# Kernel tuning notes

Measured on AMD Instinct MI355X. Metric: run time of the kernel, lower is better.

The kernel has to match this reference:

```python
import jax, jax.numpy as jnp
import numpy as np

DIM = 224   # channels, divisible by shift_size
SHIFT = 7   # shift_sizes[0]
PAD = 3     # shift_size // 2 (matches hardcoded F.pad of 3)
B, D, H, W = 2, 32, 32, 32
EPS = 1e-5


def setup_inputs() -> dict:
    key = jax.random.key(0)
    ks = jax.random.split(key, 12)
    w = lambda k: jax.random.normal(k, (DIM, DIM), jnp.float32) * 0.02
    b = lambda k: jax.random.normal(k, (DIM,), jnp.float32) * 0.02
    return {
        "x": jax.random.normal(ks[0], (B, DIM, D, H, W), jnp.float32),
        "conv1_w": w(ks[1]), "conv1_b": b(ks[2]),
        "conv21_w": w(ks[3]), "conv21_b": b(ks[4]),
        "conv22_w": w(ks[5]), "conv22_b": b(ks[6]),
        "conv23_w": w(ks[7]), "conv23_b": b(ks[8]),
        "conv3_w": w(ks[9]), "conv3_b": b(ks[10]),
        "n1_g": jnp.ones((DIM,), jnp.float32), "n1_b": jnp.zeros((DIM,), jnp.float32),
        "n2_g": jnp.ones((DIM,), jnp.float32), "n2_b": jnp.zeros((DIM,), jnp.float32),
    }


def _pw(x, w, b):
    # 1x1x1 conv3d == per-voxel channel GEMM
    return jnp.einsum('bcdhw,oc->bodhw', x, w) + b[None, :, None, None, None]


def _gn(x, g, b):
    # GroupNorm(1, C): normalize over (C,D,H,W) per sample, per-channel affine
    mu = jnp.mean(x, axis=(1, 2, 3, 4), keepdims=True)
    var = jnp.mean((x - mu) ** 2, axis=(1, 2, 3, 4), keepdims=True)
    xn = (x - mu) * jax.lax.rsqrt(var + EPS)
    return xn * g[None, :, None, None, None] + b[None, :, None, None, None]


def _pad3(x):
    return jnp.pad(x, ((0, 0), (0, 0), (PAD, PAD), (PAD, PAD), (PAD, PAD)))


def _shift_narrow(xp, axis):
    # chunk channels into SHIFT groups, roll each by -PAD..PAD along `axis`,
    # concat, then narrow each spatial dim at offset PAD to (D,H,W)
    chunks = jnp.split(xp, SHIFT, axis=1)
    rolled = [jnp.roll(c, s, axis=axis) for c, s in zip(chunks, range(-PAD, PAD + 1))]
    cat = jnp.concatenate(rolled, axis=1)
    return cat[:, :, PAD:PAD + D, PAD:PAD + H, PAD:PAD + W]


def reference(x, conv1_w, conv1_b, conv21_w, conv21_b, conv22_w, conv22_b,
              conv23_w, conv23_b, conv3_w, conv3_b, n1_g, n1_b, n2_g, n2_b):
    gelu = lambda t: jax.nn.gelu(t, approximate=False)
    x_orig = x
    h = gelu(_gn(_pw(x, conv1_w, conv1_b), n1_g, n1_b))
    # NOTE: torch code re-pads the running tensor before each axis branch,
    # while always narrowing at offset PAD — reproduced faithfully.
    xp1 = _pad3(h)                       # padded once
    x_d = gelu(_pw(_shift_narrow(xp1, 2), conv21_w, conv21_b))
    xp2 = _pad3(xp1)                     # padded twice
    x_h = gelu(_pw(_shift_narrow(xp2, 3), conv22_w, conv22_b))
    xp3 = _pad3(xp2)                     # padded thrice
    x_w = gelu(_pw(_shift_narrow(xp3, 4), conv23_w, conv23_b))
    y = _pw(_gn(x_d + x_h + x_w, n2_g, n2_b), conv3_w, conv3_b)
    return y + x_orig
```

## Files before the change

### kernel.cpp

```cpp
#include <hip/hip_runtime.h>

#define DIM 224
#define NVOX 32768
#define NBATCH 2

typedef __attribute__((ext_vector_type(8))) short bf16x8;
typedef __attribute__((ext_vector_type(4))) float f32x4;

__device__ __forceinline__ unsigned short f2bf(float f){
  unsigned int u = __builtin_bit_cast(unsigned int, f);
  u += 0x7fffu + ((u >> 16) & 1u);
  return (unsigned short)(u >> 16);
}
__device__ __forceinline__ float bf2f(unsigned short s){
  unsigned int u = ((unsigned int)s) << 16;
  return __builtin_bit_cast(float, u);
}
__device__ __forceinline__ float gelu_f(float x){
  return 0.5f * x * (1.0f + erff(x * 0.70710678118654752440f));
}

__device__ __forceinline__ void gemm_core(const unsigned short* Atile,
                                          unsigned short* Wtile,
                                          const unsigned short* __restrict__ wmat,
                                          int tid, int lane, int wm, int wn,
                                          f32x4 acc[2][7])
{
  for (int ks = 0; ks < 7; ++ks){
    if (ks) __syncthreads();
    #pragma unroll
    for (int it = 0; it < 4; ++it){
      int idx = tid + it * 256;
      if (idx < 896){
        int o = idx >> 2, kp = idx & 3;
        *(bf16x8*)&Wtile[o * 40 + kp * 8] =
            *(const bf16x8*)&wmat[o * 224 + ks * 32 + kp * 8];
      }
    }
    __syncthreads();
    bf16x8 af[2];
    #pragma unroll
    for (int m = 0; m < 2; ++m){
      int row = wm * 32 + m * 16 + (lane & 15);
      int up  = ((ks << 2) | (lane >> 4)) ^ (row & 31);
      af[m] = *(const bf16x8*)&Atile[row * 256 + up * 8];
    }
    #pragma unroll
    for (int n = 0; n < 7; ++n){
      int o = wn * 112 + n * 16 + (lane & 15);
      bf16x8 wf = *(const bf16x8*)&Wtile[o * 40 + (lane >> 4) * 8];
      acc[0][n] = __builtin_amdgcn_mfma_f32_16x16x32_bf16(af[0], wf, acc[0][n], 0, 0, 0);
      acc[1][n] = __builtin_amdgcn_mfma_f32_16x16x32_bf16(af[1], wf, acc[1][n], 0, 0, 0);
    }
  }
}

__global__ void k_wconv(const float* __restrict__ w1, const float* __restrict__ w2,
                        const float* __restrict__ w3, const float* __restrict__ w4,
                        const float* __restrict__ w5,
                        unsigned short* __restrict__ dst, float* __restrict__ stats)
{
  int i = blockIdx.x * 256 + threadIdx.x;
  if (blockIdx.x == 0 && threadIdx.x < 16) stats[threadIdx.x] = 0.f;
  if (i < 5 * DIM * DIM){
    int m = i / (DIM * DIM), r = i - m * (DIM * DIM);
    const float* s = (m == 0) ? w1 : (m == 1) ? w2 : (m == 2) ? w3 : (m == 3) ? w4 : w5;
    dst[i] = f2bf(s[r]);
  }
}

__global__ __launch_bounds__(256, 2) void k_gemm1(
    const float* __restrict__ x, const unsigned short* __restrict__ w1,
    const float* __restrict__ b1, unsigned short* __restrict__ h0,
    float* __restrict__ stats)
{
  __shared__ __align__(16) unsigned short Atile[64 * 256];
  __shared__ __align__(16) unsigned short Wtile[224 * 40];
  __shared__ float red[8];
  int tid = threadIdx.x;
  int lane = tid & 63, wid = tid >> 6;
  int wm = wid & 1, wn = wid >> 1;
  int blk = blockIdx.x;
  int b = blk >> 9;
  int vb = (blk & 511) << 6;

  {
    int v = tid & 63;
    const float* xb = x + (size_t)b * DIM * NVOX + vb + v;
    int sw = v & 31;
    for (int j0 = tid >> 6; j0 < 28; j0 += 4){
      bf16x8 pv;
      #pragma unroll
      for (int i = 0; i < 8; ++i)
        pv[i] = (short)f2bf(xb[(size_t)(j0 * 8 + i) * NVOX]);
      *(bf16x8*)&Atile[v * 256 + (j0 ^ sw) * 8] = pv;
    }
  }
  __syncthreads();

  f32x4 zz = {0.f, 0.f, 0.f, 0.f};
  f32x4 acc[2][7];
  #pragma unroll
  for (int m = 0; m < 2; ++m)
    #pragma unroll
    for (int n = 0; n < 7; ++n) acc[m][n] = zz;

  gemm_core(Atile, Wtile, w1, tid, lane, wm, wn, acc);
  __syncthreads();

  unsigned short* Ebf = Atile;
  float lsum = 0.f, lsq = 0.f;
  #pragma unroll
  for (int n = 0; n < 7; ++n){
    int col = wn * 112 + n * 16 + (lane & 15);
    float bias = b1[col];
    #pragma unroll
    for (int m = 0; m < 2; ++m){
      #pragma unroll
      for (int r = 0; r < 4; ++r){
        float val = acc[m][n][r] + bias;
        lsum += val; lsq += val * val;
        int vl = wm * 32 + m * 16 + (lane >> 4) * 4 + r;
        Ebf[vl * 224 + col] = f2bf(val);
      }
    }
  }
  #pragma unroll
  for (int off = 32; off; off >>= 1){
    lsum += __shfl_down(lsum, off);
    lsq  += __shfl_down(lsq,  off);
  }
  if (lane == 0){ red[wid * 2] = lsum; red[wid * 2 + 1] = lsq; }
  __syncthreads();
  if (tid == 0){
    atomicAdd(&stats[0 + b], red[0] + red[2] + red[4] + red[6]);
    atomicAdd(&stats[2 + b], red[1] + red[3] + red[5] + red[7]);
  }
  for (int idx = tid; idx < 64 * 28; idx += 256){
    int vl = idx / 28, u = idx - vl * 28;
    *(bf16x8*)&h0[((size_t)b * NVOX + vb + vl) * DIM + u * 8] =
        *(const bf16x8*)&Ebf[vl * 224 + u * 8];
  }
}

__global__ void k_stats(const float* __restrict__ stats, int soff,
                        const float* __restrict__ g, const float* __restrict__ be,
                        float* __restrict__ Aout, float* __restrict__ Bout)
{
  int tid = threadIdx.x;
  const float invN = 1.0f / (float)((size_t)DIM * NVOX);
  for (int i = tid; i < 2 * DIM; i += 256){
    int b = i / DIM, c = i - b * DIM;
    float mu   = stats[soff + b] * invN;
    float var  = stats[soff + 2 + b] * invN - mu * mu;
    float rstd = rsqrtf(var + 1e-5f);
    float a = rstd * g[c];
    Aout[i] = a;
    Bout[i] = be[c] - mu * a;
  }
}

__global__ void k_act(unsigned short* __restrict__ h,
                      const float* __restrict__ A1, const float* __restrict__ B1)
{
  const size_t total = (size_t)NBATCH * NVOX * 28;
  for (size_t idx = (size_t)blockIdx.x * 256 + threadIdx.x; idx < total;
       idx += (size_t)2048 * 256){
    int u = (int)(idx % 28);
    size_t bv = idx / 28;
    int b = (int)(bv >> 15);
    unsigned short* p = h + bv * DIM + u * 8;
    bf16x8 hv = *(const bf16x8*)p;
    const float* Ap = A1 + b * DIM + u * 8;
    const float* Bp = B1 + b * DIM + u * 8;
    #pragma unroll
    for (int i = 0; i < 8; ++i){
      float f = bf2f((unsigned short)hv[i]) * Ap[i] + Bp[i];
      hv[i] = (short)f2bf(gelu_f(f));
    }
    *(bf16x8*)p = hv;
  }
}

__global__ __launch_bounds__(256, 2) void k_shift(
    const unsigned short* __restrict__ h, const unsigned short* __restrict__ wall,
    const float* __restrict__ b21, const float* __restrict__ b22,
    const float* __restrict__ b23,
    unsigned short* __restrict__ sout, float* __restrict__ stats)
{
  __shared__ __align__(16) unsigned short Atile[64 * 256];
  __shared__ __align__(16) unsigned short Wtile[224 * 40];
  __shared__ float red[8];
  int tid = threadIdx.x;
  int lane = tid & 63, wid = tid >> 6;
  int wm = wid & 1, wn = wid >> 1;
  int blk = blockIdx.x;
  int b = blk >> 9;
  int vb = (blk & 511) << 6;

  f32x4 zz = {0.f, 0.f, 0.f, 0.f};
  f32x4 sacc[2][7];
  #pragma unroll
  for (int m = 0; m < 2; ++m)
    #pragma unroll
    for (int n = 0; n < 7; ++n) sacc[m][n] = zz;

  for (int cv = 0; cv < 3; ++cv){
    __syncthreads();
    #pragma unroll
    for (int it = 0; it < 8; ++it){
      int slot = tid + it * 256;
      int v = slot >> 5, up = slot & 31;
      int u = up ^ (v & 31);
      bf16x8 val = {0, 0, 0, 0, 0, 0, 0, 0};
      if (u < 28){
        int g = u >> 2;
        int vg = vb + v;
        int d = vg >> 10, hh = (vg >> 5) & 31, w = vg & 31;
        int dd, hy, wx;
        if (cv == 0){ dd = d - (g - 3); hy = hh;           wx = w; }
        else if (cv == 1){ dd = d - 3;  hy = hh - (g - 3) - 3; wx = w - 3; }
        else { dd = d - 6;              hy = hh - 6;       wx = w - (g - 3) - 6; }
        if ((unsigned)dd < 32u && (unsigned)hy < 32u && (unsigned)wx < 32u){
          size_t vsrc = ((size_t)dd << 10) + (hy << 5) + wx;
          val = *(const bf16x8*)&h[((size_t)b * NVOX + vsrc) * DIM + u * 8];
        }
      }
      *(bf16x8*)&Atile[slot * 8] = val;
    }
    __syncthreads();

    f32x4 acc[2][7];
    #pragma unroll
    for (int m = 0; m < 2; ++m)
      #pragma unroll
      for (int n = 0; n < 7; ++n) acc[m][n] = zz;

    const unsigned short* wmat = wall + (size_t)(cv + 1) * DIM * DIM;
    gemm_core(Atile, Wtile, wmat, tid, lane, wm, wn, acc);

    const float* bp = (cv == 0) ? b21 : (cv == 1) ? b22 : b23;
    #pragma unroll
    for (int n = 0; n < 7; ++n){
      float bias = bp[wn * 112 + n * 16 + (lane & 15)];
      #pragma unroll
      for (int m = 0; m < 2; ++m)
        #pragma unroll
        for (int r = 0; r < 4; ++r)
          sacc[m][n][r] += gelu_f(acc[m][n][r] + bias);
    }
  }
  __syncthreads();

  unsigned short* Ebf = Atile;
  float lsum = 0.f, lsq = 0.f;
  #pragma unroll
  for (int n = 0; n < 7; ++n){
    int col = wn * 112 + n * 16 + (lane & 15);
    #pragma unroll
    for (int m = 0; m < 2; ++m){
      #pragma unroll
      for (int r = 0; r < 4; ++r){
        float val = sacc[m][n][r];
        lsum += val; lsq += val * val;
        int vl = wm * 32 + m * 16 + (lane >> 4) * 4 + r;
        Ebf[vl * 224 + col] = f2bf(val);
      }
    }
  }
  #pragma unroll
  for (int off = 32; off; off >>= 1){
    lsum += __shfl_down(lsum, off);
    lsq  += __shfl_down(lsq,  off);
  }
  if (lane == 0){ red[wid * 2] = lsum; red[wid * 2 + 1] = lsq; }
  __syncthreads();
  if (tid == 0){
    atomicAdd(&stats[4 + b], red[0] + red[2] + red[4] + red[6]);
    atomicAdd(&stats[6 + b], red[1] + red[3] + red[5] + red[7]);
  }
  for (int idx = tid; idx < 64 * 28; idx += 256){
    int vl = idx / 28, u = idx - vl * 28;
    *(bf16x8*)&sout[((size_t)b * NVOX + vb + vl) * DIM + u * 8] =
        *(const bf16x8*)&Ebf[vl * 224 + u * 8];
  }
}

__global__ __launch_bounds__(256, 2) void k_out(
    const unsigned short* __restrict__ sbf, const unsigned short* __restrict__ w3,
    const float* __restrict__ b3,
    const float* __restrict__ A2, const float* __restrict__ B2,
    const float* __restrict__ xorig, float* __restrict__ y)
{
  __shared__ __align__(16) unsigned short Atile[64 * 256];
  __shared__ __align__(16) unsigned short Wtile[224 * 40];
  int tid = threadIdx.x;
  int lane = tid & 63, wid = tid >> 6;
  int wm = wid & 1, wn = wid >> 1;
  int blk = blockIdx.x;
  int b = blk >> 9;
  int vb = (blk & 511) << 6;

  #pragma unroll
  for (int it = 0; it < 8; ++it){
    int slot = tid + it * 256;
    int v = slot >> 5, up = slot & 31;
    int u = up ^ (v & 31);
    bf16x8 val = {0, 0, 0, 0, 0, 0, 0, 0};
    if (u < 28){
      bf16x8 sv = *(const bf16x8*)&sbf[((size_t)b * NVOX + vb + v) * DIM + u * 8];
      const float* Ap = A2 + b * DIM + u * 8;
      const float* Bp = B2 + b * DIM + u * 8;
      #pragma unroll
      for (int i = 0; i < 8; ++i)
        val[i] = (short)f2bf(bf2f((unsigned short)sv[i]) * Ap[i] + Bp[i]);
    }
    *(bf16x8*)&Atile[slot * 8] = val;
  }
  __syncthreads();

  f32x4 zz = {0.f, 0.f, 0.f, 0.f};
  f32x4 acc[2][7];
  #pragma unroll
  for (int m = 0; m < 2; ++m)
    #pragma unroll
    for (int n = 0; n < 7; ++n) acc[m][n] = zz;

  gemm_core(Atile, Wtile, w3, tid, lane, wm, wn, acc);

  float bias[7];
  #pragma unroll
  for (int n = 0; n < 7; ++n) bias[n] = b3[wn * 112 + n * 16 + (lane & 15)];

  float* Et = (float*)Atile;
  for (int half = 0; half < 2; ++half){
    __syncthreads();
    if (wn == half){
      #pragma unroll
      for (int m = 0; m < 2; ++m)
        #pragma unroll
        for (int n = 0; n < 7; ++n)
          #pragma unroll
          for (int r = 0; r < 4; ++r){
            int ol = n * 16 + (lane & 15);
            int vl = wm * 32 + m * 16 + (lane >> 4) * 4 + r;
            Et[ol * 65 + vl] = acc[m][n][r] + bias[n];
          }
    }
    __syncthreads();
    int v = tid & 63;
    for (int row = tid >> 6; row < 112; row += 4){
      int o = half * 112 + row;
      size_t gi = ((size_t)b * DIM + o) * NVOX + vb + v;
      y[gi] = Et[row * 65 + v] + xorig[gi];
    }
  }
}

extern "C" void kernel_launch(void* const* d_in, const int* in_sizes, int n_in,
                              void* d_out, int out_size, void* d_ws, size_t ws_size,
                              hipStream_t stream)
{
  const float* x    = (const float*)d_in[0];
  const float* w1f  = (const float*)d_in[1];
  const float* b1   = (const float*)d_in[2];
  const float* w21f = (const float*)d_in[3];
  const float* b21  = (const float*)d_in[4];
  const float* w22f = (const float*)d_in[5];
  const float* b22  = (const float*)d_in[6];
  const float* w23f = (const float*)d_in[7];
  const float* b23  = (const float*)d_in[8];
  const float* w3f  = (const float*)d_in[9];
  const float* b3   = (const float*)d_in[10];
  const float* n1g  = (const float*)d_in[11];
  const float* n1b  = (const float*)d_in[12];
  const float* n2g  = (const float*)d_in[13];
  const float* n2b  = (const float*)d_in[14];
  float* y = (float*)d_out;

  float* stats = (float*)d_ws;
  float* A1 = stats + 16; float* B1 = A1 + 448;
  float* A2 = B1 + 448;   float* B2 = A2 + 448;
  unsigned short* Wbf = (unsigned short*)((char*)d_ws + 8192);
  unsigned short* sbf = (unsigned short*)((char*)d_ws + 524288);
  unsigned short* hbf = (unsigned short*)d_out;

  k_wconv<<<980, 256, 0, stream>>>(w1f, w21f, w22f, w23f, w3f, Wbf, stats);
  k_gemm1<<<1024, 256, 0, stream>>>(x, Wbf, b1, hbf, stats);
  k_stats<<<1, 256, 0, stream>>>(stats, 0, n1g, n1b, A1, B1);
  k_act<<<2048, 256, 0, stream>>>(hbf, A1, B1);
  k_shift<<<1024, 256, 0, stream>>>(hbf, Wbf, b21, b22, b23, sbf, stats);
  k_stats<<<1, 256, 0, stream>>>(stats, 4, n2g, n2b, A2, B2);
  k_out<<<1024, 256, 0, stream>>>(sbf, Wbf + 4 * DIM * DIM, b3, A2, B2, x, y);
}
```

Measured before the change: 426.8 us.

## Keep weight fragments in registers, split output channels, double-buffer tiles, fast GELU

Each GEMM kernel now assigns every block a 64-channel slice of the output and a run of voxel tiles. Weight fragments are held in registers instead of being restaged through LDS on each k-step, and the next activation tile is loaded while the current one is processed with double-buffered LDS. The second GroupNorm's affine is folded into the conv3 weights and bias, and erf-GELU is replaced by a tanh approximation built on __expf. These changes raise register pressure and recompute the input gather once per channel slice, and the GELU approximation changes numerics slightly.

```diff
diff --git a/kernel.cpp b/kernel.cpp
--- a/kernel.cpp
+++ b/kernel.cpp
@@ -2,10 +2,10 @@
 
 #define DIM 224
 #define NVOX 32768
-#define NBATCH 2
 
 typedef __attribute__((ext_vector_type(8))) short bf16x8;
 typedef __attribute__((ext_vector_type(4))) float f32x4;
+typedef unsigned short ushort_t;
 
 __device__ __forceinline__ unsigned short f2bf(float f){
   unsigned int u = __builtin_bit_cast(unsigned int, f);
@@ -16,49 +16,50 @@
   unsigned int u = ((unsigned int)s) << 16;
   return __builtin_bit_cast(float, u);
 }
-__device__ __forceinline__ float gelu_f(float x){
-  return 0.5f * x * (1.0f + erff(x * 0.70710678118654752440f));
-}
-
-__device__ __forceinline__ void gemm_core(const unsigned short* Atile,
-                                          unsigned short* Wtile,
-                                          const unsigned short* __restrict__ wmat,
-                                          int tid, int lane, int wm, int wn,
-                                          f32x4 acc[2][7])
-{
-  for (int ks = 0; ks < 7; ++ks){
-    if (ks) __syncthreads();
-    #pragma unroll
-    for (int it = 0; it < 4; ++it){
-      int idx = tid + it * 256;
-      if (idx < 896){
-        int o = idx >> 2, kp = idx & 3;
-        *(bf16x8*)&Wtile[o * 40 + kp * 8] =
-            *(const bf16x8*)&wmat[o * 224 + ks * 32 + kp * 8];
-      }
-    }
-    __syncthreads();
-    bf16x8 af[2];
-    #pragma unroll
-    for (int m = 0; m < 2; ++m){
-      int row = wm * 32 + m * 16 + (lane & 15);
-      int up  = ((ks << 2) | (lane >> 4)) ^ (row & 31);
-      af[m] = *(const bf16x8*)&Atile[row * 256 + up * 8];
-    }
-    #pragma unroll
-    for (int n = 0; n < 7; ++n){
-      int o = wn * 112 + n * 16 + (lane & 15);
-      bf16x8 wf = *(const bf16x8*)&Wtile[o * 40 + (lane >> 4) * 8];
-      acc[0][n] = __builtin_amdgcn_mfma_f32_16x16x32_bf16(af[0], wf, acc[0][n], 0, 0, 0);
-      acc[1][n] = __builtin_amdgcn_mfma_f32_16x16x32_bf16(af[1], wf, acc[1][n], 0, 0, 0);
-    }
+__device__ __forceinline__ float gelu_fast(float x){
+  float t = 0.7978845608028654f * (x + 0.044715f * x * x * x);
+  float e = __expf(2.0f * t);
+  float th = 1.0f - 2.0f / (e + 1.0f);
+  return 0.5f * x * (1.0f + th);
+}
+
+__device__ __forceinline__ void load_wf(bf16x8 wf[4][7], const ushort_t* __restrict__ wm,
+                                        int ob, int lane, int nv)
+{
+  bf16x8 zz = {0,0,0,0,0,0,0,0};
+  #pragma unroll
+  for (int n = 0; n < 4; ++n)
+    #pragma unroll
+    for (int ks = 0; ks < 7; ++ks)
+      wf[n][ks] = (n < nv)
+        ? *(const bf16x8*)&wm[(size_t)(ob + n*16 + (lane & 15)) * 224 + ks*32 + (lane >> 4)*8]
+        : zz;
+}
+
+__device__ __forceinline__ void gather7(const ushort_t* __restrict__ h, int b, int vb,
+                                        int cv, const int* sv, const int* su, bf16x8* gr)
+{
+  #pragma unroll
+  for (int i = 0; i < 7; ++i){
+    int v = sv[i], u = su[i];
+    int g = u >> 2;
+    int vg = vb + v;
+    int d = vg >> 10, hh = (vg >> 5) & 31, w = vg & 31;
+    int dd, hy, wx;
+    if (cv == 0){ dd = d - (g - 3); hy = hh;               wx = w; }
+    else if (cv == 1){ dd = d - 3;  hy = hh - (g - 3) - 3; wx = w - 3; }
+    else { dd = d - 6;              hy = hh - 6;           wx = w - (g - 3) - 6; }
+    bf16x8 val = {0,0,0,0,0,0,0,0};
+    if ((unsigned)dd < 32u && (unsigned)hy < 32u && (unsigned)wx < 32u)
+      val = *(const bf16x8*)&h[(((size_t)b << 15) + (size_t)((dd << 10) + (hy << 5) + wx)) * 224 + u*8];
+    gr[i] = val;
   }
 }
 
 __global__ void k_wconv(const float* __restrict__ w1, const float* __restrict__ w2,
                         const float* __restrict__ w3, const float* __restrict__ w4,
                         const float* __restrict__ w5,
-                        unsigned short* __restrict__ dst, float* __restrict__ stats)
+                        ushort_t* __restrict__ dst, float* __restrict__ stats)
 {
   int i = blockIdx.x * 256 + threadIdx.x;
   if (blockIdx.x == 0 && threadIdx.x < 16) stats[threadIdx.x] = 0.f;
@@ -70,59 +71,96 @@
 }
 
 __global__ __launch_bounds__(256, 2) void k_gemm1(
-    const float* __restrict__ x, const unsigned short* __restrict__ w1,
-    const float* __restrict__ b1, unsigned short* __restrict__ h0,
-    float* __restrict__ stats)
-{
-  __shared__ __align__(16) unsigned short Atile[64 * 256];
-  __shared__ __align__(16) unsigned short Wtile[224 * 40];
+    const float* __restrict__ x, const ushort_t* __restrict__ w1,
+    const float* __restrict__ b1, ushort_t* __restrict__ h0, float* __restrict__ stats)
+{
+  __shared__ __align__(16) ushort_t Abuf[2][64 * 232];
   __shared__ float red[8];
-  int tid = threadIdx.x;
-  int lane = tid & 63, wid = tid >> 6;
-  int wm = wid & 1, wn = wid >> 1;
-  int blk = blockIdx.x;
-  int b = blk >> 9;
-  int vb = (blk & 511) << 6;
+  int tid = threadIdx.x, lane = tid & 63, wid = tid >> 6;
+  int task = ((blockIdx.x & 7) << 7) | (blockIdx.x >> 3);
+  int nh = task & 3, tg = task >> 2;
+  int ob = nh << 6;
+  int nv = (ob == 192) ? 2 : 4;
+  int tile0 = tg * 4;
+  int b = tile0 >> 9;
+
+  bf16x8 wf[4][7];
+  load_wf(wf, w1, ob, lane, nv);
+  float bias[4];
+  #pragma unroll
+  for (int n = 0; n < 4; ++n)
+    bias[n] = (n < nv) ? b1[ob + n*16 + (lane & 15)] : 0.f;
 
   {
+    int vb = (tile0 & 511) << 6;
+    const float* xp = x + ((size_t)b * 224) * 32768 + vb + (tid & 63);
     int v = tid & 63;
-    const float* xb = x + (size_t)b * DIM * NVOX + vb + v;
-    int sw = v & 31;
-    for (int j0 = tid >> 6; j0 < 28; j0 += 4){
+    #pragma unroll
+    for (int i = 0; i < 7; ++i){
+      int u = (tid >> 6) + i * 4;
       bf16x8 pv;
       #pragma unroll
-      for (int i = 0; i < 8; ++i)
-        pv[i] = (short)f2bf(xb[(size_t)(j0 * 8 + i) * NVOX]);
-      *(bf16x8*)&Atile[v * 256 + (j0 ^ sw) * 8] = pv;
-    }
-  }
-  __syncthreads();
-
-  f32x4 zz = {0.f, 0.f, 0.f, 0.f};
-  f32x4 acc[2][7];
-  #pragma unroll
-  for (int m = 0; m < 2; ++m)
-    #pragma unroll
-    for (int n = 0; n < 7; ++n) acc[m][n] = zz;
-
-  gemm_core(Atile, Wtile, w1, tid, lane, wm, wn, acc);
-  __syncthreads();
-
-  unsigned short* Ebf = Atile;
+      for (int j = 0; j < 8; ++j) pv[j] = (short)f2bf(xp[(size_t)(u*8 + j) * 32768]);
+      *(bf16x8*)&Abuf[0][v * 232 + u * 8] = pv;
+    }
+  }
+  __syncthreads();
+
   float lsum = 0.f, lsq = 0.f;
-  #pragma unroll
-  for (int n = 0; n < 7; ++n){
-    int col = wn * 112 + n * 16 + (lane & 15);
-    float bias = b1[col];
-    #pragma unroll
-    for (int m = 0; m < 2; ++m){
+  f32x4 zz = {0.f,0.f,0.f,0.f};
+
+  for (int t = 0; t < 4; ++t){
+    int tile = tile0 + t;
+    int vb = (tile & 511) << 6;
+    float xr[7][8];
+    if (t < 3){
+      int vb2 = ((tile + 1) & 511) << 6;
+      const float* xp = x + ((size_t)b * 224) * 32768 + vb2 + (tid & 63);
+      #pragma unroll
+      for (int i = 0; i < 7; ++i){
+        int u = (tid >> 6) + i * 4;
+        #pragma unroll
+        for (int j = 0; j < 8; ++j) xr[i][j] = xp[(size_t)(u*8 + j) * 32768];
+      }
+    }
+    f32x4 acc[4] = {zz, zz, zz, zz};
+    const ushort_t* A = Abuf[t & 1];
+    #pragma unroll
+    for (int ks = 0; ks < 7; ++ks){
+      bf16x8 af = *(const bf16x8*)&A[(wid*16 + (lane & 15)) * 232 + (ks*4 + (lane >> 4)) * 8];
+      #pragma unroll
+      for (int n = 0; n < 4; ++n)
+        acc[n] = __builtin_amdgcn_mfma_f32_16x16x32_bf16(af, wf[n][ks], acc[n], 0, 0, 0);
+    }
+    __syncthreads();
+    if (t < 3){
+      int v = tid & 63;
+      #pragma unroll
+      for (int i = 0; i < 7; ++i){
+        int u = (tid >> 6) + i * 4;
+        bf16x8 pv;
+        #pragma unroll
+        for (int j = 0; j < 8; ++j) pv[j] = (short)f2bf(xr[i][j]);
+        *(bf16x8*)&Abuf[(t + 1) & 1][v * 232 + u * 8] = pv;
+      }
+    }
+    ushort_t* Ebf = (ushort_t*)Abuf[t & 1];
+    #pragma unroll
+    for (int n = 0; n < 4; ++n)
       #pragma unroll
       for (int r = 0; r < 4; ++r){
-        float val = acc[m][n][r] + bias;
+        float val = acc[n][r] + bias[n];
         lsum += val; lsq += val * val;
-        int vl = wm * 32 + m * 16 + (lane >> 4) * 4 + r;
-        Ebf[vl * 224 + col] = f2bf(val);
-      }
+        Ebf[(wid*16 + (lane >> 4)*4 + r) * 72 + n*16 + (lane & 15)] = f2bf(val);
+      }
+    __syncthreads();
+    size_t base = (((size_t)b << 15) + vb) * 224 + ob;
+    #pragma unroll
+    for (int i = 0; i < 2; ++i){
+      int slot = tid + i * 256;
+      int v = slot >> 3, u = slot & 7;
+      if (ob + u*8 < 224)
+        *(bf16x8*)&h0[base + (size_t)v * 224 + u * 8] = *(const bf16x8*)&Ebf[v * 72 + u * 8];
     }
   }
   #pragma unroll
@@ -130,16 +168,11 @@
     lsum += __shfl_down(lsum, off);
     lsq  += __shfl_down(lsq,  off);
   }
-  if (lane == 0){ red[wid * 2] = lsum; red[wid * 2 + 1] = lsq; }
+  if (lane == 0){ red[wid*2] = lsum; red[wid*2 + 1] = lsq; }
   __syncthreads();
   if (tid == 0){
     atomicAdd(&stats[0 + b], red[0] + red[2] + red[4] + red[6]);
     atomicAdd(&stats[2 + b], red[1] + red[3] + red[5] + red[7]);
-  }
-  for (int idx = tid; idx < 64 * 28; idx += 256){
-    int vl = idx / 28, u = idx - vl * 28;
-    *(bf16x8*)&h0[((size_t)b * NVOX + vb + vl) * DIM + u * 8] =
-        *(const bf16x8*)&Ebf[vl * 224 + u * 8];
   }
 }
 
@@ -160,112 +193,119 @@
   }
 }
 
-__global__ void k_act(unsigned short* __restrict__ h,
+__global__ void k_act(ushort_t* __restrict__ h,
                       const float* __restrict__ A1, const float* __restrict__ B1)
 {
-  const size_t total = (size_t)NBATCH * NVOX * 28;
+  const size_t total = (size_t)2 * NVOX * 28;
   for (size_t idx = (size_t)blockIdx.x * 256 + threadIdx.x; idx < total;
        idx += (size_t)2048 * 256){
     int u = (int)(idx % 28);
     size_t bv = idx / 28;
     int b = (int)(bv >> 15);
-    unsigned short* p = h + bv * DIM + u * 8;
+    ushort_t* p = h + bv * 224 + u * 8;
     bf16x8 hv = *(const bf16x8*)p;
-    const float* Ap = A1 + b * DIM + u * 8;
-    const float* Bp = B1 + b * DIM + u * 8;
+    const float* Ap = A1 + b * 224 + u * 8;
+    const float* Bp = B1 + b * 224 + u * 8;
     #pragma unroll
     for (int i = 0; i < 8; ++i){
       float f = bf2f((unsigned short)hv[i]) * Ap[i] + Bp[i];
-      hv[i] = (short)f2bf(gelu_f(f));
+      hv[i] = (short)f2bf(gelu_fast(f));
     }
     *(bf16x8*)p = hv;
   }
 }
 
 __global__ __launch_bounds__(256, 2) void k_shift(
-    const unsigned short* __restrict__ h, const unsigned short* __restrict__ wall,
+    const ushort_t* __restrict__ h, const ushort_t* __restrict__ wall,
     const float* __restrict__ b21, const float* __restrict__ b22,
     const float* __restrict__ b23,
-    unsigned short* __restrict__ sout, float* __restrict__ stats)
-{
-  __shared__ __align__(16) unsigned short Atile[64 * 256];
-  __shared__ __align__(16) unsigned short Wtile[224 * 40];
+    ushort_t* __restrict__ sout, float* __restrict__ stats)
+{
+  __shared__ __align__(16) ushort_t Abuf[2][64 * 232];
   __shared__ float red[8];
-  int tid = threadIdx.x;
-  int lane = tid & 63, wid = tid >> 6;
-  int wm = wid & 1, wn = wid >> 1;
-  int blk = blockIdx.x;
-  int b = blk >> 9;
-  int vb = (blk & 511) << 6;
-
-  f32x4 zz = {0.f, 0.f, 0.f, 0.f};
-  f32x4 sacc[2][7];
-  #pragma unroll
-  for (int m = 0; m < 2; ++m)
-    #pragma unroll
-    for (int n = 0; n < 7; ++n) sacc[m][n] = zz;
-
-  for (int cv = 0; cv < 3; ++cv){
+  int tid = threadIdx.x, lane = tid & 63, wid = tid >> 6;
+  int task = ((blockIdx.x & 7) << 8) | (blockIdx.x >> 3);
+  int nh = task & 3, tg = task >> 2;
+  int ob = nh << 6;
+  int nv = (ob == 192) ? 2 : 4;
+  int tile0 = tg * 2;
+  int b = tile0 >> 9;
+  int sv[7], su[7];
+  #pragma unroll
+  for (int i = 0; i < 7; ++i){ int s = tid + i*256; sv[i] = (s * 9363) >> 18; su[i] = s - sv[i] * 28; }
+
+  float biasv[3][4];
+  #pragma unroll
+  for (int n = 0; n < 4; ++n){
+    int o = ob + n*16 + (lane & 15);
+    biasv[0][n] = (n < nv) ? b21[o] : 0.f;
+    biasv[1][n] = (n < nv) ? b22[o] : 0.f;
+    biasv[2][n] = (n < nv) ? b23[o] : 0.f;
+  }
+
+  bf16x8 wf[4][7];
+  load_wf(wf, wall + (size_t)1 * 224 * 224, ob, lane, nv);
+  bf16x8 gr[7];
+  gather7(h, b, (tile0 & 511) << 6, 0, sv, su, gr);
+  #pragma unroll
+  for (int i = 0; i < 7; ++i) *(bf16x8*)&Abuf[0][sv[i]*232 + su[i]*8] = gr[i];
+  __syncthreads();
+
+  f32x4 zz = {0.f,0.f,0.f,0.f};
+  f32x4 sacc[2][4] = {{zz,zz,zz,zz},{zz,zz,zz,zz}};
+
+  #pragma unroll
+  for (int s = 0; s < 6; ++s){
+    const int cv = s >> 1, tl = s & 1;
+    if (s < 5)
+      gather7(h, b, ((tile0 + ((s + 1) & 1)) & 511) << 6, (s + 1) >> 1, sv, su, gr);
+    f32x4 acc[4] = {zz, zz, zz, zz};
+    const ushort_t* A = Abuf[tl];
+    #pragma unroll
+    for (int ks = 0; ks < 7; ++ks){
+      bf16x8 af = *(const bf16x8*)&A[(wid*16 + (lane & 15)) * 232 + (ks*4 + (lane >> 4)) * 8];
+      #pragma unroll
+      for (int n = 0; n < 4; ++n)
+        acc[n] = __builtin_amdgcn_mfma_f32_16x16x32_bf16(af, wf[n][ks], acc[n], 0, 0, 0);
+    }
+    #pragma unroll
+    for (int n = 0; n < 4; ++n)
+      #pragma unroll
+      for (int r = 0; r < 4; ++r)
+        sacc[tl][n][r] += gelu_fast(acc[n][r] + biasv[cv][n]);
+    if (tl == 1 && cv < 2)
+      load_wf(wf, wall + (size_t)(2 + cv) * 224 * 224, ob, lane, nv);
+    if (s < 5){
+      #pragma unroll
+      for (int i = 0; i < 7; ++i) *(bf16x8*)&Abuf[(s + 1) & 1][sv[i]*232 + su[i]*8] = gr[i];
+    }
     __syncthreads();
-    #pragma unroll
-    for (int it = 0; it < 8; ++it){
-      int slot = tid + it * 256;
-      int v = slot >> 5, up = slot & 31;
-      int u = up ^ (v & 31);
-      bf16x8 val = {0, 0, 0, 0, 0, 0, 0, 0};
-      if (u < 28){
-        int g = u >> 2;
-        int vg = vb + v;
-        int d = vg >> 10, hh = (vg >> 5) & 31, w = vg & 31;
-        int dd, hy, wx;
-        if (cv == 0){ dd = d - (g - 3); hy = hh;           wx = w; }
-        else if (cv == 1){ dd = d - 3;  hy = hh - (g - 3) - 3; wx = w - 3; }
-        else { dd = d - 6;              hy = hh - 6;       wx = w - (g - 3) - 6; }
-        if ((unsigned)dd < 32u && (unsigned)hy < 32u && (unsigned)wx < 32u){
-          size_t vsrc = ((size_t)dd << 10) + (hy << 5) + wx;
-          val = *(const bf16x8*)&h[((size_t)b * NVOX + vsrc) * DIM + u * 8];
-        }
-      }
-      *(bf16x8*)&Atile[slot * 8] = val;
-    }
-    __syncthreads();
-
-    f32x4 acc[2][7];
-    #pragma unroll
-    for (int m = 0; m < 2; ++m)
-      #pragma unroll
-      for (int n = 0; n < 7; ++n) acc[m][n] = zz;
-
-    const unsigned short* wmat = wall + (size_t)(cv + 1) * DIM * DIM;
-    gemm_core(Atile, Wtile, wmat, tid, lane, wm, wn, acc);
-
-    const float* bp = (cv == 0) ? b21 : (cv == 1) ? b22 : b23;
-    #pragma unroll
-    for (int n = 0; n < 7; ++n){
-      float bias = bp[wn * 112 + n * 16 + (lane & 15)];
-      #pragma unroll
-      for (int m = 0; m < 2; ++m)
-        #pragma unroll
-        for (int r = 0; r < 4; ++r)
-          sacc[m][n][r] += gelu_f(acc[m][n][r] + bias);
-    }
-  }
-  __syncthreads();
-
-  unsigned short* Ebf = Atile;
+  }
+
   float lsum = 0.f, lsq = 0.f;
   #pragma unroll
-  for (int n = 0; n < 7; ++n){
-    int col = wn * 112 + n * 16 + (lane & 15);
-    #pragma unroll
-    for (int m = 0; m < 2; ++m){
+  for (int tl = 0; tl < 2; ++tl){
+    ushort_t* Ebf = (ushort_t*)Abuf[tl];
+    #pragma unroll
+    for (int n = 0; n < 4; ++n)
       #pragma unroll
       for (int r = 0; r < 4; ++r){
-        float val = sacc[m][n][r];
+        float val = sacc[tl][n][r];
         lsum += val; lsq += val * val;
-        int vl = wm * 32 + m * 16 + (lane >> 4) * 4 + r;
-        Ebf[vl * 224 + col] = f2bf(val);
-      }
+        Ebf[(wid*16 + (lane >> 4)*4 + r) * 72 + n*16 + (lane & 15)] = f2bf(val);
+      }
+  }
+  __syncthreads();
+  #pragma unroll
+  for (int tl = 0; tl < 2; ++tl){
+    const ushort_t* Ebf = (const ushort_t*)Abuf[tl];
+    size_t base = (((size_t)b << 15) + (((tile0 + tl) & 511) << 6)) * 224 + ob;
+    #pragma unroll
+    for (int i = 0; i < 2; ++i){
+      int slot = tid + i * 256;
+      int v = slot >> 3, u = slot & 7;
+      if (ob + u*8 < 224)
+        *(bf16x8*)&sout[base + (size_t)v * 224 + u * 8] = *(const bf16x8*)&Ebf[v * 72 + u * 8];
     }
   }
   #pragma unroll
@@ -273,86 +313,120 @@
     lsum += __shfl_down(lsum, off);
     lsq  += __shfl_down(lsq,  off);
   }
-  if (lane == 0){ red[wid * 2] = lsum; red[wid * 2 + 1] = lsq; }
+  if (lane == 0){ red[wid*2] = lsum; red[wid*2 + 1] = lsq; }
   __syncthreads();
   if (tid == 0){
     atomicAdd(&stats[4 + b], red[0] + red[2] + red[4] + red[6]);
     atomicAdd(&stats[6 + b], red[1] + red[3] + red[5] + red[7]);
   }
-  for (int idx = tid; idx < 64 * 28; idx += 256){
-    int vl = idx / 28, u = idx - vl * 28;
-    *(bf16x8*)&sout[((size_t)b * NVOX + vb + vl) * DIM + u * 8] =
-        *(const bf16x8*)&Ebf[vl * 224 + u * 8];
-  }
 }
 
 __global__ __launch_bounds__(256, 2) void k_out(
-    const unsigned short* __restrict__ sbf, const unsigned short* __restrict__ w3,
+    const ushort_t* __restrict__ sbf, const ushort_t* __restrict__ w3,
     const float* __restrict__ b3,
     const float* __restrict__ A2, const float* __restrict__ B2,
     const float* __restrict__ xorig, float* __restrict__ y)
 {
-  __shared__ __align__(16) unsigned short Atile[64 * 256];
-  __shared__ __align__(16) unsigned short Wtile[224 * 40];
-  int tid = threadIdx.x;
-  int lane = tid & 63, wid = tid >> 6;
-  int wm = wid & 1, wn = wid >> 1;
-  int blk = blockIdx.x;
-  int b = blk >> 9;
-  int vb = (blk & 511) << 6;
-
-  #pragma unroll
-  for (int it = 0; it < 8; ++it){
-    int slot = tid + it * 256;
-    int v = slot >> 5, up = slot & 31;
-    int u = up ^ (v & 31);
-    bf16x8 val = {0, 0, 0, 0, 0, 0, 0, 0};
-    if (u < 28){
-      bf16x8 sv = *(const bf16x8*)&sbf[((size_t)b * NVOX + vb + v) * DIM + u * 8];
-      const float* Ap = A2 + b * DIM + u * 8;
-      const float* Bp = B2 + b * DIM + u * 8;
-      #pragma unroll
-      for (int i = 0; i < 8; ++i)
-        val[i] = (short)f2bf(bf2f((unsigned short)sv[i]) * Ap[i] + Bp[i]);
-    }
-    *(bf16x8*)&Atile[slot * 8] = val;
-  }
-  __syncthreads();
-
-  f32x4 zz = {0.f, 0.f, 0.f, 0.f};
-  f32x4 acc[2][7];
-  #pragma unroll
-  for (int m = 0; m < 2; ++m)
-    #pragma unroll
-    for (int n = 0; n < 7; ++n) acc[m][n] = zz;
-
-  gemm_core(Atile, Wtile, w3, tid, lane, wm, wn, acc);
-
-  float bias[7];
-  #pragma unroll
-  for (int n = 0; n < 7; ++n) bias[n] = b3[wn * 112 + n * 16 + (lane & 15)];
-
-  float* Et = (float*)Atile;
-  for (int half = 0; half < 2; ++half){
+  __shared__ __align__(16) ushort_t Abuf[2][64 * 232];
+  int tid = threadIdx.x, lane = tid & 63, wid = tid >> 6;
+  int task = ((blockIdx.x & 7) << 7) | (blockIdx.x >> 3);
+  int nh = task & 3, tg = task >> 2;
+  int ob = nh << 6;
+  int nv = (ob == 192) ? 2 : 4;
+  int tile0 = tg * 4;
+  int b = tile0 >> 9;
+  int sv[7], su[7];
+  #pragma unroll
+  for (int i = 0; i < 7; ++i){ int s = tid + i*256; sv[i] = (s * 9363) >> 18; su[i] = s - sv[i] * 28; }
+
+  bf16x8 wf[4][7];
+  load_wf(wf, w3, ob, lane, nv);
+  float bsum[4] = {0.f, 0.f, 0.f, 0.f};
+  {
+    const float* A2p = A2 + b * 224;
+    const float* B2p = B2 + b * 224;
+    #pragma unroll
+    for (int ks = 0; ks < 7; ++ks){
+      int k0 = ks*32 + (lane >> 4)*8;
+      float av[8], bv[8];
+      #pragma unroll
+      for (int j = 0; j < 8; ++j){ av[j] = A2p[k0 + j]; bv[j] = B2p[k0 + j]; }
+      #pragma unroll
+      for (int n = 0; n < 4; ++n){
+        if (n < nv){
+          bf16x8 wv = wf[n][ks];
+          #pragma unroll
+          for (int j = 0; j < 8; ++j){
+            float f = bf2f((unsigned short)wv[j]);
+            bsum[n] += f * bv[j];
+            wv[j] = (short)f2bf(f * av[j]);
+          }
+          wf[n][ks] = wv;
+        }
+      }
+    }
+  }
+  float bias[4];
+  #pragma unroll
+  for (int n = 0; n < 4; ++n){
+    float s0 = bsum[n];
+    s0 += __shfl_xor(s0, 16);
+    s0 += __shfl_xor(s0, 32);
+    bias[n] = (n < nv) ? b3[ob + n*16 + (lane & 15)] + s0 : 0.f;
+  }
+
+  {
+    int vb = (tile0 & 511) << 6;
+    #pragma unroll
+    for (int i = 0; i < 7; ++i){
+      bf16x8 val = *(const bf16x8*)&sbf[(((size_t)b << 15) + vb + sv[i]) * 224 + su[i]*8];
+      *(bf16x8*)&Abuf[0][sv[i]*232 + su[i]*8] = val;
+    }
+  }
+  __syncthreads();
+
+  f32x4 zz = {0.f,0.f,0.f,0.f};
+  bf16x8 gr[7];
+  for (int t = 0; t < 4; ++t){
+    int tile = tile0 + t;
+    int vb = (tile & 511) << 6;
+    if (t < 3){
+      int vb2 = ((tile + 1) & 511) << 6;
+      #pragma unroll
+      for (int i = 0; i < 7; ++i)
+        gr[i] = *(const bf16x8*)&sbf[(((size_t)b << 15) + vb2 + sv[i]) * 224 + su[i]*8];
+    }
+    f32x4 acc[4] = {zz, zz, zz, zz};
+    const ushort_t* A = Abuf[t & 1];
+    #pragma unroll
+    for (int ks = 0; ks < 7; ++ks){
+      bf16x8 af = *(const bf16x8*)&A[(wid*16 + (lane & 15)) * 232 + (ks*4 + (lane >> 4)) * 8];
+      #pragma unroll
+      for (int n = 0; n < 4; ++n)
+        acc[n] = __builtin_amdgcn_mfma_f32_16x16x32_bf16(af, wf[n][ks], acc[n], 0, 0, 0);
+    }
     __syncthreads();
-    if (wn == half){
-      #pragma unroll
-      for (int m = 0; m < 2; ++m)
-        #pragma unroll
-        for (int n = 0; n < 7; ++n)
-          #pragma unroll
-          for (int r = 0; r < 4; ++r){
-            int ol = n * 16 + (lane & 15);
-            int vl = wm * 32 + m * 16 + (lane >> 4) * 4 + r;
-            Et[ol * 65 + vl] = acc[m][n][r] + bias[n];
-          }
-    }
+    if (t < 3){
+      #pragma unroll
+      for (int i = 0; i < 7; ++i)
+        *(bf16x8*)&Abuf[(t + 1) & 1][sv[i]*232 + su[i]*8] = gr[i];
+    }
+    float* Et = (float*)Abuf[t & 1];
+    #pragma unroll
+    for (int n = 0; n < 4; ++n)
+      #pragma unroll
+      for (int r = 0; r < 4; ++r)
+        Et[(n*16 + (lane & 15)) * 66 + wid*16 + (lane >> 4)*4 + r] = acc[n][r] + bias[n];
     __syncthreads();
     int v = tid & 63;
-    for (int row = tid >> 6; row < 112; row += 4){
-      int o = half * 112 + row;
-      size_t gi = ((size_t)b * DIM + o) * NVOX + vb + v;
-      y[gi] = Et[row * 65 + v] + xorig[gi];
+    size_t gbase = (((size_t)b * 224 + ob) << 15) + vb + v;
+    #pragma unroll
+    for (int i = 0; i < 16; ++i){
+      int row = (tid >> 6) + i * 4;
+      if (ob + row < 224){
+        size_t gi = gbase + ((size_t)row << 15);
+        y[gi] = Et[row * 66 + v] + xorig[gi];
+      }
     }
   }
 }
@@ -381,15 +455,15 @@
   float* stats = (float*)d_ws;
   float* A1 = stats + 16; float* B1 = A1 + 448;
   float* A2 = B1 + 448;   float* B2 = A2 + 448;
-  unsigned short* Wbf = (unsigned short*)((char*)d_ws + 8192);
-  unsigned short* sbf = (unsigned short*)((char*)d_ws + 524288);
-  unsigned short* hbf = (unsigned short*)d_out;
+  ushort_t* Wbf = (ushort_t*)((char*)d_ws + 8192);
+  ushort_t* sbf = (ushort_t*)((char*)d_ws + 524288);
+  ushort_t* hbf = (ushort_t*)d_out;
 
   k_wconv<<<980, 256, 0, stream>>>(w1f, w21f, w22f, w23f, w3f, Wbf, stats);
   k_gemm1<<<1024, 256, 0, stream>>>(x, Wbf, b1, hbf, stats);
   k_stats<<<1, 256, 0, stream>>>(stats, 0, n1g, n1b, A1, B1);
   k_act<<<2048, 256, 0, stream>>>(hbf, A1, B1);
-  k_shift<<<1024, 256, 0, stream>>>(hbf, Wbf, b21, b22, b23, sbf, stats);
+  k_shift<<<2048, 256, 0, stream>>>(hbf, Wbf, b21, b22, b23, sbf, stats);
   k_stats<<<1, 256, 0, stream>>>(stats, 4, n2g, n2b, A2, B2);
   k_out<<<1024, 256, 0, stream>>>(sbf, Wbf + 4 * DIM * DIM, b3, A2, B2, x, y);
 }
```

Measured after the change: 347.8 us. 1.23x faster.
